# Performance work log

Measured on AMD Instinct MI355X. Metric: run time of the kernel, lower is better.

Reference implementation:

```python
import jax, jax.numpy as jnp
import numpy as np

N_NODES = 50000
N_EDGES = 800000
HID = 256
EDGE_DIM = 3


def setup_inputs() -> dict:
    key = jax.random.key(0)
    ks = jax.random.split(key, 10)
    h = jax.random.normal(ks[0], (N_NODES, HID), dtype=jnp.float32)
    edge_index = jax.random.randint(ks[1], (2, N_EDGES), 0, N_NODES, dtype=jnp.int64)
    edge_attr = jax.random.normal(ks[2], (N_EDGES, EDGE_DIM), dtype=jnp.float32)
    # edge_mlp: Linear(3, hid//2) -> SiLU -> Linear(hid//2, 1)
    half = HID // 2
    W1 = jax.random.normal(ks[3], (EDGE_DIM, half), dtype=jnp.float32) / np.sqrt(EDGE_DIM)
    b1 = jnp.zeros((half,), dtype=jnp.float32)
    W2 = jax.random.normal(ks[4], (half, 1), dtype=jnp.float32) / np.sqrt(half)
    b2 = jnp.zeros((1,), dtype=jnp.float32)
    # GCNConv lin (bias=False inside lin; separate additive bias)
    Wc = jax.random.normal(ks[5], (HID, HID), dtype=jnp.float32) / np.sqrt(HID)
    bc = jnp.zeros((HID,), dtype=jnp.float32)
    return {"h": h, "edge_index": edge_index, "edge_attr": edge_attr,
            "W1": W1, "b1": b1, "W2": W2, "b2": b2, "Wc": Wc, "bc": bc}


def reference(h, edge_index, edge_attr, W1, b1, W2, b2, Wc, bc):
    N = h.shape[0]
    # per-edge scalar weight in (0,1): sigmoid(MLP(edge_attr))
    t = jax.nn.silu(edge_attr @ W1 + b1)
    w = jax.nn.sigmoid((t @ W2 + b2)[:, 0])  # [E]

    # add self loops with weight 1.0
    loop = jnp.arange(N, dtype=edge_index.dtype)
    row = jnp.concatenate([edge_index[0], loop])  # sources
    col = jnp.concatenate([edge_index[1], loop])  # targets
    ew = jnp.concatenate([w, jnp.ones((N,), dtype=w.dtype)])

    # symmetric normalization (PyG gcn_norm, flow source_to_target)
    deg = jax.ops.segment_sum(ew, col, num_segments=N)
    dinv = jnp.where(deg > 0, jax.lax.rsqrt(deg), 0.0)
    norm = dinv[row] * ew * dinv[col]  # [E+N]

    # linear transform then gather-scale-scatter aggregation
    x = h @ Wc  # [N, HID]
    msg = x[row] * norm[:, None]  # [E+N, HID]
    out = jax.ops.segment_sum(msg, col, num_segments=N) + bc
    return out
```

## Files before the change

### kernel.cpp

```cpp
#include <hip/hip_runtime.h>

#define NN 50000
#define NE 800000
#define HID 256
#define HALF 128
#define CAP 48
#define MT ((NN + 63) / 64)
#define EPT 2
#define MLPB ((NE + 256 * EPT - 1) / (256 * EPT))

typedef __attribute__((ext_vector_type(8))) short short8;
typedef __attribute__((ext_vector_type(4))) float floatx4;

#define WSCALE 1.52587890625e-5f

__device__ inline unsigned short f2b(float f) {
    unsigned int u = __float_as_uint(f);
    return (unsigned short)((u + 0x7FFFu + ((u >> 16) & 1u)) >> 16);
}
__device__ inline float b2f(unsigned int u) { return __uint_as_float(u << 16); }

__device__ inline float fsigmoid(float x) {
    return __builtin_amdgcn_rcpf(1.0f + __expf(-x));
}

__global__ __launch_bounds__(256) void k_prep(const float* __restrict__ Wc,
                                              unsigned short* __restrict__ Wt,
                                              uint4* __restrict__ zb) {
    int t = blockIdx.x * 256 + threadIdx.x;
    if (t < 12500) zb[t] = make_uint4(0u, 0u, 0u, 0u);
    int n = t >> 8, k = t & 255;
    Wt[n * 256 + k] = f2b(Wc[k * 256 + n]);
}

__global__ __launch_bounds__(256, 6) void k_mlp_fill(
    const float* __restrict__ ea, const int* __restrict__ eidx,
    const float* __restrict__ W1, const float* __restrict__ b1,
    const float* __restrict__ W2, const float* __restrict__ b2,
    unsigned int* __restrict__ cnt, unsigned int* __restrict__ epk) {
    __shared__ float4 wp[HALF];
    __shared__ __align__(16) float w2s[HALF];
    int tid = threadIdx.x;
    int e0 = blockIdx.x * (256 * EPT) + tid;
    int row[EPT], col[EPT];
    float a0[EPT], a1[EPT], a2[EPT];
    bool ok[EPT];
#pragma unroll
    for (int i = 0; i < EPT; ++i) {
        int ei = e0 + i * 256;
        ok[i] = ei < NE;
        int ec = ok[i] ? ei : (NE - 1);
        row[i] = eidx[ec];
        col[i] = eidx[NE + ec];
        a0[i] = ea[3 * ec];
        a1[i] = ea[3 * ec + 1];
        a2[i] = ea[3 * ec + 2];
    }
    if (tid < HALF) {
        wp[tid] = make_float4(W1[tid], W1[HALF + tid], W1[2 * HALF + tid], b1[tid]);
        w2s[tid] = W2[tid];
    }
    __syncthreads();
    unsigned slot[EPT];
#pragma unroll
    for (int i = 0; i < EPT; ++i)
        slot[i] = ok[i] ? atomicAdd(&cnt[col[i]], 1u) : 0xFFFFFFFFu;
    float acc[EPT] = {0.f, 0.f};
#pragma unroll 1
    for (int g = 0; g < HALF / 4; ++g) {
        int j = g * 4;
        float4 w0 = wp[j], w1 = wp[j + 1], w2v = wp[j + 2], w3 = wp[j + 3];
        float4 v2 = *(const float4*)&w2s[j];
#pragma unroll
        for (int i = 0; i < EPT; ++i) {
            float t0 = fmaf(a0[i], w0.x, fmaf(a1[i], w0.y, fmaf(a2[i], w0.z, w0.w)));
            float t1 = fmaf(a0[i], w1.x, fmaf(a1[i], w1.y, fmaf(a2[i], w1.z, w1.w)));
            float t2 = fmaf(a0[i], w2v.x, fmaf(a1[i], w2v.y, fmaf(a2[i], w2v.z, w2v.w)));
            float t3 = fmaf(a0[i], w3.x, fmaf(a1[i], w3.y, fmaf(a2[i], w3.z, w3.w)));
            float s0 = t0 * fsigmoid(t0);
            float s1 = t1 * fsigmoid(t1);
            float s2 = t2 * fsigmoid(t2);
            float s3 = t3 * fsigmoid(t3);
            acc[i] = fmaf(s0, v2.x, fmaf(s1, v2.y, fmaf(s2, v2.z, fmaf(s3, v2.w, acc[i]))));
        }
    }
    float bb = b2[0];
#pragma unroll
    for (int i = 0; i < EPT; ++i) {
        float wv = fsigmoid(acc[i] + bb);
        unsigned q = __float2uint_rn(wv * 65536.0f);
        if (q > 65535u) q = 65535u;
        if (ok[i] && slot[i] < CAP)
            epk[col[i] * CAP + slot[i]] = (unsigned)row[i] | (q << 16);
    }
}

__global__ __launch_bounds__(256) void k_gemm_deg(
    const float* __restrict__ A, const unsigned short* __restrict__ Wt,
    const unsigned int* __restrict__ cnt, const uint4* __restrict__ epk4,
    float* __restrict__ dinv, unsigned short* __restrict__ xs) {
    __shared__ __align__(16) unsigned short As[8 * 64 * 40];
    __shared__ float dinvs[64];
    int tid = threadIdx.x;
    int wave = tid >> 6, lane = tid & 63;
    int mbase = blockIdx.x * 64, nbase = wave * 64;
    int lrow = lane & 15, lg = lane >> 4;
    int srow = tid >> 2, skg = tid & 3;
    int arow = mbase + srow;
    if (arow >= NN) arow = NN - 1;
    const float* Ap = A + (size_t)arow * HID + skg * 8;

    if (tid < 64) {
        int drow = mbase + tid;
        bool vw = drow < NN;
        if (!vw) drow = NN - 1;
        int dcn = (int)cnt[drow];
        if (dcn > CAP) dcn = CAP;
        const uint4* dbp = epk4 + (size_t)drow * (CAP / 4);
        unsigned s = 0;
#pragma unroll
        for (int i = 0; i < CAP / 4; ++i) {
            uint4 qv = dbp[i];
            int k0 = i * 4;
            s += (k0 + 0 < dcn) ? (qv.x >> 16) : 0u;
            s += (k0 + 1 < dcn) ? (qv.y >> 16) : 0u;
            s += (k0 + 2 < dcn) ? (qv.z >> 16) : 0u;
            s += (k0 + 3 < dcn) ? (qv.w >> 16) : 0u;
        }
        float dv = rsqrtf(fmaf((float)s, WSCALE, 1.0f));
        dinvs[tid] = dv;
        if (vw) dinv[mbase + tid] = dv;
    }

#define PACKST(c, f0, f1) { uint4 pk;                                   \
    pk.x = (unsigned)f2b(f0.x) | ((unsigned)f2b(f0.y) << 16);           \
    pk.y = (unsigned)f2b(f0.z) | ((unsigned)f2b(f0.w) << 16);           \
    pk.z = (unsigned)f2b(f1.x) | ((unsigned)f2b(f1.y) << 16);           \
    pk.w = (unsigned)f2b(f1.z) | ((unsigned)f2b(f1.w) << 16);           \
    *(uint4*)&As[(c) * 2560 + srow * 40 + skg * 8] = pk; }

#pragma unroll
    for (int g = 0; g < 2; ++g) {
        int c0 = g * 4;
        float4 fa0 = *(const float4*)(Ap + (c0 + 0) * 32);
        float4 fb0 = *(const float4*)(Ap + (c0 + 0) * 32 + 4);
        float4 fa1 = *(const float4*)(Ap + (c0 + 1) * 32);
        float4 fb1 = *(const float4*)(Ap + (c0 + 1) * 32 + 4);
        float4 fa2 = *(const float4*)(Ap + (c0 + 2) * 32);
        float4 fb2 = *(const float4*)(Ap + (c0 + 2) * 32 + 4);
        float4 fa3 = *(const float4*)(Ap + (c0 + 3) * 32);
        float4 fb3 = *(const float4*)(Ap + (c0 + 3) * 32 + 4);
        PACKST(c0 + 0, fa0, fb0);
        PACKST(c0 + 1, fa1, fb1);
        PACKST(c0 + 2, fa2, fb2);
        PACKST(c0 + 3, fa3, fb3);
    }
    __syncthreads();

    floatx4 acc[4][4];
#pragma unroll
    for (int t = 0; t < 4; ++t)
#pragma unroll
        for (int u = 0; u < 4; ++u)
            acc[t][u] = (floatx4){0.f, 0.f, 0.f, 0.f};

#pragma unroll
    for (int c = 0; c < 8; ++c) {
        short8 af[4], bf[4];
#pragma unroll
        for (int t = 0; t < 4; ++t)
            af[t] = *(const short8*)&As[c * 2560 + (t * 16 + lrow) * 40 + lg * 8];
#pragma unroll
        for (int u = 0; u < 4; ++u)
            bf[u] = *(const short8*)&Wt[(nbase + u * 16 + lrow) * 256 + c * 32 + lg * 8];
#pragma unroll
        for (int t = 0; t < 4; ++t)
#pragma unroll
            for (int u = 0; u < 4; ++u)
                acc[t][u] = __builtin_amdgcn_mfma_f32_16x16x32_bf16(
                    af[t], bf[u], acc[t][u], 0, 0, 0);
    }
#pragma unroll
    for (int t = 0; t < 4; ++t) {
        int rowb = mbase + t * 16 + lg * 4;
#pragma unroll
        for (int r = 0; r < 4; ++r) {
            int row = rowb + r;
            if (row < NN) {
                float di = dinvs[t * 16 + lg * 4 + r];
#pragma unroll
                for (int u = 0; u < 4; ++u)
                    xs[row * 256 + nbase + u * 16 + lrow] = f2b(acc[t][u][r] * di);
            }
        }
    }
}

__global__ __launch_bounds__(256) void k_aggregate(
    const unsigned short* __restrict__ xs, const unsigned int* __restrict__ cnt,
    const float* __restrict__ dinv, const unsigned int* __restrict__ epk,
    const float* __restrict__ bc, float* __restrict__ out) {
    int n = blockIdx.x * 4 + (threadIdx.x >> 6);
    int lane = threadIdx.x & 63;
    if (n >= NN) return;
    int c4 = lane * 4;
    int cn = (int)cnt[n];
    if (cn > CAP) cn = CAP;
    float di = dinv[n];
    ushort4 xv = *(const ushort4*)&xs[n * 256 + c4];
    float ax = b2f(xv.x), ay = b2f(xv.y), az = b2f(xv.z), aw = b2f(xv.w);

    const uint4* bp = (const uint4*)(epk + n * CAP);
    int nb = (cn + 7) >> 3;
    uint4 qa = bp[0], qb = bp[1];
    for (int b = 0; b < nb; ++b) {
        int k0 = b * 8;
        int i2 = 2 * b + 2;
        if (i2 > 10) i2 = 10;
        uint4 qa2 = bp[i2], qb2 = bp[i2 + 1];
        unsigned p0 = (k0 + 0 < cn) ? qa.x : 0u;
        unsigned p1 = (k0 + 1 < cn) ? qa.y : 0u;
        unsigned p2 = (k0 + 2 < cn) ? qa.z : 0u;
        unsigned p3 = (k0 + 3 < cn) ? qa.w : 0u;
        unsigned p4 = (k0 + 4 < cn) ? qb.x : 0u;
        unsigned p5 = (k0 + 5 < cn) ? qb.y : 0u;
        unsigned p6 = (k0 + 6 < cn) ? qb.z : 0u;
        unsigned p7 = (k0 + 7 < cn) ? qb.w : 0u;
        ushort4 v0 = *(const ushort4*)&xs[(p0 & 0xFFFFu) * 256 + c4];
        ushort4 v1 = *(const ushort4*)&xs[(p1 & 0xFFFFu) * 256 + c4];
        ushort4 v2 = *(const ushort4*)&xs[(p2 & 0xFFFFu) * 256 + c4];
        ushort4 v3 = *(const ushort4*)&xs[(p3 & 0xFFFFu) * 256 + c4];
        ushort4 v4 = *(const ushort4*)&xs[(p4 & 0xFFFFu) * 256 + c4];
        ushort4 v5 = *(const ushort4*)&xs[(p5 & 0xFFFFu) * 256 + c4];
        ushort4 v6 = *(const ushort4*)&xs[(p6 & 0xFFFFu) * 256 + c4];
        ushort4 v7 = *(const ushort4*)&xs[(p7 & 0xFFFFu) * 256 + c4];
        float n0 = (float)(p0 >> 16) * WSCALE;
        float n1 = (float)(p1 >> 16) * WSCALE;
        float n2 = (float)(p2 >> 16) * WSCALE;
        float n3 = (float)(p3 >> 16) * WSCALE;
        float n4 = (float)(p4 >> 16) * WSCALE;
        float n5 = (float)(p5 >> 16) * WSCALE;
        float n6 = (float)(p6 >> 16) * WSCALE;
        float n7 = (float)(p7 >> 16) * WSCALE;
        ax = fmaf(b2f(v0.x), n0, ax); ay = fmaf(b2f(v0.y), n0, ay);
        az = fmaf(b2f(v0.z), n0, az); aw = fmaf(b2f(v0.w), n0, aw);
        ax = fmaf(b2f(v1.x), n1, ax); ay = fmaf(b2f(v1.y), n1, ay);
        az = fmaf(b2f(v1.z), n1, az); aw = fmaf(b2f(v1.w), n1, aw);
        ax = fmaf(b2f(v2.x), n2, ax); ay = fmaf(b2f(v2.y), n2, ay);
        az = fmaf(b2f(v2.z), n2, az); aw = fmaf(b2f(v2.w), n2, aw);
        ax = fmaf(b2f(v3.x), n3, ax); ay = fmaf(b2f(v3.y), n3, ay);
        az = fmaf(b2f(v3.z), n3, az); aw = fmaf(b2f(v3.w), n3, aw);
        ax = fmaf(b2f(v4.x), n4, ax); ay = fmaf(b2f(v4.y), n4, ay);
        az = fmaf(b2f(v4.z), n4, az); aw = fmaf(b2f(v4.w), n4, aw);
        ax = fmaf(b2f(v5.x), n5, ax); ay = fmaf(b2f(v5.y), n5, ay);
        az = fmaf(b2f(v5.z), n5, az); aw = fmaf(b2f(v5.w), n5, aw);
        ax = fmaf(b2f(v6.x), n6, ax); ay = fmaf(b2f(v6.y), n6, ay);
        az = fmaf(b2f(v6.z), n6, az); aw = fmaf(b2f(v6.w), n6, aw);
        ax = fmaf(b2f(v7.x), n7, ax); ay = fmaf(b2f(v7.y), n7, ay);
        az = fmaf(b2f(v7.z), n7, az); aw = fmaf(b2f(v7.w), n7, aw);
        qa = qa2; qb = qb2;
    }
    float4 bv = *(const float4*)&bc[c4];
    float4 res;
    res.x = fmaf(ax, di, bv.x);
    res.y = fmaf(ay, di, bv.y);
    res.z = fmaf(az, di, bv.z);
    res.w = fmaf(aw, di, bv.w);
    *(float4*)&out[n * 256 + c4] = res;
}

extern "C" void kernel_launch(void* const* d_in, const int* in_sizes, int n_in,
                              void* d_out, int out_size, void* d_ws, size_t ws_size,
                              hipStream_t stream) {
    const float* h   = (const float*)d_in[0];
    const int* eidx  = (const int*)d_in[1];
    const float* ea  = (const float*)d_in[2];
    const float* W1  = (const float*)d_in[3];
    const float* b1  = (const float*)d_in[4];
    const float* W2  = (const float*)d_in[5];
    const float* b2  = (const float*)d_in[6];
    const float* Wc  = (const float*)d_in[7];
    const float* bc  = (const float*)d_in[8];
    float* out = (float*)d_out;

    char* p = (char*)d_ws;
    unsigned int* cnt  = (unsigned int*)p;   p += (size_t)NN * 4;
    float* dinv        = (float*)p;          p += (size_t)NN * 4;
    unsigned int* epk  = (unsigned int*)p;   p += (size_t)NN * CAP * 4;
    unsigned short* xs = (unsigned short*)p; p += (size_t)NN * HID * 2;
    unsigned short* Wt = (unsigned short*)p;

    k_prep<<<256, 256, 0, stream>>>(Wc, Wt, (uint4*)cnt);
    k_mlp_fill<<<MLPB, 256, 0, stream>>>(ea, eidx, W1, b1, W2, b2, cnt, epk);
    k_gemm_deg<<<MT, 256, 0, stream>>>(h, Wt, cnt, (const uint4*)epk, dinv, xs);
    k_aggregate<<<(NN + 3) / 4, 256, 0, stream>>>(xs, cnt, dinv, epk, bc, out);
}
```

Before: 255.6 us.

## Pad per-node counters to 64B, recompute dinv in aggregate, fully unroll gather

Each node's atomic in-degree counter now sits in its own 64-byte slot, so atomics from different nodes no longer share a cache line. The prep kernel zeroes this larger array using more blocks. The aggregate kernel stops reading a dinv buffer. It recomputes the degree sum from the packed edge weights it already loads, so the gemm kernel no longer writes dinv to global memory. The aggregation loop becomes fully unrolled 16-edge chunks with early exit, which issues more gathers in flight. The cost is 16x more counter memory to zero and higher register pressure in aggregate.

```diff
diff --git a/kernel.cpp b/kernel.cpp
--- a/kernel.cpp
+++ b/kernel.cpp
@@ -8,6 +8,7 @@
 #define MT ((NN + 63) / 64)
 #define EPT 2
 #define MLPB ((NE + 256 * EPT - 1) / (256 * EPT))
+#define NPREPB 782
 
 typedef __attribute__((ext_vector_type(8))) short short8;
 typedef __attribute__((ext_vector_type(4))) float floatx4;
@@ -28,16 +29,18 @@
                                               unsigned short* __restrict__ Wt,
                                               uint4* __restrict__ zb) {
     int t = blockIdx.x * 256 + threadIdx.x;
-    if (t < 12500) zb[t] = make_uint4(0u, 0u, 0u, 0u);
-    int n = t >> 8, k = t & 255;
-    Wt[n * 256 + k] = f2b(Wc[k * 256 + n]);
+    if (t < 200000) zb[t] = make_uint4(0u, 0u, 0u, 0u);
+    if (t < 65536) {
+        int n = t >> 8, k = t & 255;
+        Wt[n * 256 + k] = f2b(Wc[k * 256 + n]);
+    }
 }
 
 __global__ __launch_bounds__(256, 6) void k_mlp_fill(
     const float* __restrict__ ea, const int* __restrict__ eidx,
     const float* __restrict__ W1, const float* __restrict__ b1,
     const float* __restrict__ W2, const float* __restrict__ b2,
-    unsigned int* __restrict__ cnt, unsigned int* __restrict__ epk) {
+    unsigned int* __restrict__ cntp, unsigned int* __restrict__ epk) {
     __shared__ float4 wp[HALF];
     __shared__ __align__(16) float w2s[HALF];
     int tid = threadIdx.x;
@@ -64,7 +67,7 @@
     unsigned slot[EPT];
 #pragma unroll
     for (int i = 0; i < EPT; ++i)
-        slot[i] = ok[i] ? atomicAdd(&cnt[col[i]], 1u) : 0xFFFFFFFFu;
+        slot[i] = ok[i] ? atomicAdd(&cntp[col[i] * 16], 1u) : 0xFFFFFFFFu;
     float acc[EPT] = {0.f, 0.f};
 #pragma unroll 1
     for (int g = 0; g < HALF / 4; ++g) {
@@ -97,8 +100,8 @@
 
 __global__ __launch_bounds__(256) void k_gemm_deg(
     const float* __restrict__ A, const unsigned short* __restrict__ Wt,
-    const unsigned int* __restrict__ cnt, const uint4* __restrict__ epk4,
-    float* __restrict__ dinv, unsigned short* __restrict__ xs) {
+    const unsigned int* __restrict__ cntp, const uint4* __restrict__ epk4,
+    unsigned short* __restrict__ xs) {
     __shared__ __align__(16) unsigned short As[8 * 64 * 40];
     __shared__ float dinvs[64];
     int tid = threadIdx.x;
@@ -112,9 +115,8 @@
 
     if (tid < 64) {
         int drow = mbase + tid;
-        bool vw = drow < NN;
-        if (!vw) drow = NN - 1;
-        int dcn = (int)cnt[drow];
+        if (drow >= NN) drow = NN - 1;
+        int dcn = (int)cntp[drow * 16];
         if (dcn > CAP) dcn = CAP;
         const uint4* dbp = epk4 + (size_t)drow * (CAP / 4);
         unsigned s = 0;
@@ -127,9 +129,7 @@
             s += (k0 + 2 < dcn) ? (qv.z >> 16) : 0u;
             s += (k0 + 3 < dcn) ? (qv.w >> 16) : 0u;
         }
-        float dv = rsqrtf(fmaf((float)s, WSCALE, 1.0f));
-        dinvs[tid] = dv;
-        if (vw) dinv[mbase + tid] = dv;
+        dinvs[tid] = rsqrtf(fmaf((float)s, WSCALE, 1.0f));
     }
 
 #define PACKST(c, f0, f1) { uint4 pk;                                   \
@@ -196,70 +196,56 @@
     }
 }
 
-__global__ __launch_bounds__(256) void k_aggregate(
-    const unsigned short* __restrict__ xs, const unsigned int* __restrict__ cnt,
-    const float* __restrict__ dinv, const unsigned int* __restrict__ epk,
-    const float* __restrict__ bc, float* __restrict__ out) {
+#define CH16(W0, W1, W2, W3, BASE)                                          \
+    {                                                                       \
+        unsigned pp[16];                                                    \
+        pp[0] = W0.x; pp[1] = W0.y; pp[2] = W0.z; pp[3] = W0.w;             \
+        pp[4] = W1.x; pp[5] = W1.y; pp[6] = W1.z; pp[7] = W1.w;             \
+        pp[8] = W2.x; pp[9] = W2.y; pp[10] = W2.z; pp[11] = W2.w;           \
+        pp[12] = W3.x; pp[13] = W3.y; pp[14] = W3.z; pp[15] = W3.w;         \
+        _Pragma("unroll")                                                   \
+        for (int k = 0; k < 16; ++k)                                        \
+            if ((BASE) + k >= cn) pp[k] = 0u;                               \
+        ushort4 vv[16];                                                     \
+        _Pragma("unroll")                                                   \
+        for (int k = 0; k < 16; ++k)                                        \
+            vv[k] = *(const ushort4*)&xs[(pp[k] & 0xFFFFu) * 256 + c4];     \
+        _Pragma("unroll")                                                   \
+        for (int k = 0; k < 16; ++k) {                                      \
+            unsigned qw = pp[k] >> 16;                                      \
+            s += qw;                                                        \
+            float nk = (float)qw * WSCALE;                                  \
+            ax = fmaf(b2f(vv[k].x), nk, ax); ay = fmaf(b2f(vv[k].y), nk, ay); \
+            az = fmaf(b2f(vv[k].z), nk, az); aw = fmaf(b2f(vv[k].w), nk, aw); \
+        }                                                                   \
+    }
+
+__global__ __launch_bounds__(256, 4) void k_aggregate(
+    const unsigned short* __restrict__ xs, const unsigned int* __restrict__ cntp,
+    const unsigned int* __restrict__ epk, const float* __restrict__ bc,
+    float* __restrict__ out) {
     int n = blockIdx.x * 4 + (threadIdx.x >> 6);
     int lane = threadIdx.x & 63;
     if (n >= NN) return;
     int c4 = lane * 4;
-    int cn = (int)cnt[n];
+    int cn = (int)cntp[n * 16];
     if (cn > CAP) cn = CAP;
-    float di = dinv[n];
+    const uint4* bp = (const uint4*)(epk + (size_t)n * CAP);
+    uint4 A0 = bp[0], A1 = bp[1], A2 = bp[2], A3 = bp[3];
     ushort4 xv = *(const ushort4*)&xs[n * 256 + c4];
     float ax = b2f(xv.x), ay = b2f(xv.y), az = b2f(xv.z), aw = b2f(xv.w);
-
-    const uint4* bp = (const uint4*)(epk + n * CAP);
-    int nb = (cn + 7) >> 3;
-    uint4 qa = bp[0], qb = bp[1];
-    for (int b = 0; b < nb; ++b) {
-        int k0 = b * 8;
-        int i2 = 2 * b + 2;
-        if (i2 > 10) i2 = 10;
-        uint4 qa2 = bp[i2], qb2 = bp[i2 + 1];
-        unsigned p0 = (k0 + 0 < cn) ? qa.x : 0u;
-        unsigned p1 = (k0 + 1 < cn) ? qa.y : 0u;
-        unsigned p2 = (k0 + 2 < cn) ? qa.z : 0u;
-        unsigned p3 = (k0 + 3 < cn) ? qa.w : 0u;
-        unsigned p4 = (k0 + 4 < cn) ? qb.x : 0u;
-        unsigned p5 = (k0 + 5 < cn) ? qb.y : 0u;
-        unsigned p6 = (k0 + 6 < cn) ? qb.z : 0u;
-        unsigned p7 = (k0 + 7 < cn) ? qb.w : 0u;
-        ushort4 v0 = *(const ushort4*)&xs[(p0 & 0xFFFFu) * 256 + c4];
-        ushort4 v1 = *(const ushort4*)&xs[(p1 & 0xFFFFu) * 256 + c4];
-        ushort4 v2 = *(const ushort4*)&xs[(p2 & 0xFFFFu) * 256 + c4];
-        ushort4 v3 = *(const ushort4*)&xs[(p3 & 0xFFFFu) * 256 + c4];
-        ushort4 v4 = *(const ushort4*)&xs[(p4 & 0xFFFFu) * 256 + c4];
-        ushort4 v5 = *(const ushort4*)&xs[(p5 & 0xFFFFu) * 256 + c4];
-        ushort4 v6 = *(const ushort4*)&xs[(p6 & 0xFFFFu) * 256 + c4];
-        ushort4 v7 = *(const ushort4*)&xs[(p7 & 0xFFFFu) * 256 + c4];
-        float n0 = (float)(p0 >> 16) * WSCALE;
-        float n1 = (float)(p1 >> 16) * WSCALE;
-        float n2 = (float)(p2 >> 16) * WSCALE;
-        float n3 = (float)(p3 >> 16) * WSCALE;
-        float n4 = (float)(p4 >> 16) * WSCALE;
-        float n5 = (float)(p5 >> 16) * WSCALE;
-        float n6 = (float)(p6 >> 16) * WSCALE;
-        float n7 = (float)(p7 >> 16) * WSCALE;
-        ax = fmaf(b2f(v0.x), n0, ax); ay = fmaf(b2f(v0.y), n0, ay);
-        az = fmaf(b2f(v0.z), n0, az); aw = fmaf(b2f(v0.w), n0, aw);
-        ax = fmaf(b2f(v1.x), n1, ax); ay = fmaf(b2f(v1.y), n1, ay);
-        az = fmaf(b2f(v1.z), n1, az); aw = fmaf(b2f(v1.w), n1, aw);
-        ax = fmaf(b2f(v2.x), n2, ax); ay = fmaf(b2f(v2.y), n2, ay);
-        az = fmaf(b2f(v2.z), n2, az); aw = fmaf(b2f(v2.w), n2, aw);
-        ax = fmaf(b2f(v3.x), n3, ax); ay = fmaf(b2f(v3.y), n3, ay);
-        az = fmaf(b2f(v3.z), n3, az); aw = fmaf(b2f(v3.w), n3, aw);
-        ax = fmaf(b2f(v4.x), n4, ax); ay = fmaf(b2f(v4.y), n4, ay);
-        az = fmaf(b2f(v4.z), n4, az); aw = fmaf(b2f(v4.w), n4, aw);
-        ax = fmaf(b2f(v5.x), n5, ax); ay = fmaf(b2f(v5.y), n5, ay);
-        az = fmaf(b2f(v5.z), n5, az); aw = fmaf(b2f(v5.w), n5, aw);
-        ax = fmaf(b2f(v6.x), n6, ax); ay = fmaf(b2f(v6.y), n6, ay);
-        az = fmaf(b2f(v6.z), n6, az); aw = fmaf(b2f(v6.w), n6, aw);
-        ax = fmaf(b2f(v7.x), n7, ax); ay = fmaf(b2f(v7.y), n7, ay);
-        az = fmaf(b2f(v7.z), n7, az); aw = fmaf(b2f(v7.w), n7, aw);
-        qa = qa2; qb = qb2;
-    }
+    unsigned s = 0;
+
+    CH16(A0, A1, A2, A3, 0);
+    if (cn > 16) {
+        uint4 B0 = bp[4], B1 = bp[5], B2 = bp[6], B3 = bp[7];
+        CH16(B0, B1, B2, B3, 16);
+        if (cn > 32) {
+            uint4 C0 = bp[8], C1 = bp[9], C2 = bp[10], C3 = bp[11];
+            CH16(C0, C1, C2, C3, 32);
+        }
+    }
+    float di = rsqrtf(fmaf((float)s, WSCALE, 1.0f));
     float4 bv = *(const float4*)&bc[c4];
     float4 res;
     res.x = fmaf(ax, di, bv.x);
@@ -284,14 +270,13 @@
     float* out = (float*)d_out;
 
     char* p = (char*)d_ws;
-    unsigned int* cnt  = (unsigned int*)p;   p += (size_t)NN * 4;
-    float* dinv        = (float*)p;          p += (size_t)NN * 4;
+    unsigned int* cntp = (unsigned int*)p;   p += (size_t)NN * 16 * 4;
     unsigned int* epk  = (unsigned int*)p;   p += (size_t)NN * CAP * 4;
     unsigned short* xs = (unsigned short*)p; p += (size_t)NN * HID * 2;
     unsigned short* Wt = (unsigned short*)p;
 
-    k_prep<<<256, 256, 0, stream>>>(Wc, Wt, (uint4*)cnt);
-    k_mlp_fill<<<MLPB, 256, 0, stream>>>(ea, eidx, W1, b1, W2, b2, cnt, epk);
-    k_gemm_deg<<<MT, 256, 0, stream>>>(h, Wt, cnt, (const uint4*)epk, dinv, xs);
-    k_aggregate<<<(NN + 3) / 4, 256, 0, stream>>>(xs, cnt, dinv, epk, bc, out);
-}
+    k_prep<<<NPREPB, 256, 0, stream>>>(Wc, Wt, (uint4*)cntp);
+    k_mlp_fill<<<MLPB, 256, 0, stream>>>(ea, eidx, W1, b1, W2, b2, cntp, epk);
+    k_gemm_deg<<<MT, 256, 0, stream>>>(h, Wt, cntp, (const uint4*)epk, xs);
+    k_aggregate<<<(NN + 3) / 4, 256, 0, stream>>>(xs, cntp, epk, bc, out);
+}
```

Result: no change. 254.5 us (median of 2 runs) (-0.5%).
